# Optimization experiments

Measured on AMD Instinct MI355X. Metric: run time of the kernel, lower is better.

The kernel has to match this reference:

```python
import jax, jax.numpy as jnp
import numpy as np

B, T = 64, 2048
ENC_DIM, ATT_DIM, RNN_DIM, N_FILT, KSIZE, WIN = 512, 128, 1024, 32, 31, 32


def setup_inputs() -> dict:
    key = jax.random.key(0)
    ks = jax.random.split(key, 10)
    return {
        "attention_hidden_state": jax.random.normal(ks[0], (B, RNN_DIM), jnp.float32),
        "memory": jax.random.normal(ks[1], (B, T, ENC_DIM), jnp.float32),
        "processed_memory": jax.random.normal(ks[2], (B, T, ATT_DIM), jnp.float32),
        "attention_weights_cat": jax.random.uniform(ks[3], (B, 2, T), jnp.float32),
        "mask": jnp.zeros((B, T), jnp.bool_),
        "memory_lengths": jax.random.randint(ks[4], (B,), 0, T, jnp.int32),
        "current_pos": jax.random.uniform(ks[5], (B,), jnp.float32),
        "loc_conv_w": jax.random.normal(ks[6], (N_FILT, 2, KSIZE), jnp.float32) * 0.1,
        "loc_dense_w": jax.random.normal(ks[7], (ATT_DIM, N_FILT), jnp.float32) * 0.1,
        "query_w": jax.random.normal(ks[8], (ATT_DIM, RNN_DIM), jnp.float32) * 0.03,
        "v_w": jax.random.normal(ks[9], (1, ATT_DIM), jnp.float32) * 0.1,
        "pos_offset": jnp.zeros((1,), jnp.float32),
    }


def reference(attention_hidden_state, memory, processed_memory, attention_weights_cat,
              mask, memory_lengths, current_pos,
              loc_conv_w, loc_dense_w, query_w, v_w, pos_offset):
    Bn, Tn, _ = memory.shape
    pad = (KSIZE - 1) // 2
    # location conv: [B,2,T] -> [B,n_filters,T]
    conv = jax.lax.conv_general_dilated(
        attention_weights_cat, loc_conv_w, window_strides=(1,),
        padding=[(pad, pad)], dimension_numbers=("NCH", "OIH", "NCH"))
    # location dense + query projection + processed memory (fused add)
    processed = (jnp.einsum("bft,af->bta", conv, loc_dense_w)
                 + (attention_hidden_state @ query_w.T)[:, None, :]
                 + processed_memory)                      # [B,T,att_dim]
    alignment = jnp.tanh(processed) @ v_w[0]              # [B,T]
    # dynamic windowed mask around current_pos
    cp = current_pos + pos_offset[0]
    max_end = (memory_lengths - 1 - WIN).astype(cp.dtype)
    cp = jnp.minimum(jnp.maximum(cp, jnp.float32(WIN)), max_end)
    mask_start = jnp.round(jnp.maximum(cp - WIN, 0.0))
    mask_end = mask_start + 2 * WIN
    pos = jnp.arange(Tn, dtype=cp.dtype)
    pos_mask = (pos[None, :] >= mask_start[:, None]) & (pos[None, :] <= mask_end[:, None])
    full_mask = mask | ~pos_mask
    alignment = jnp.where(full_mask, jnp.float32(-1e9), alignment)
    attention_weights = jax.nn.softmax(alignment, axis=1)  # [B,T]
    attention_context = jnp.einsum("bt,btd->bd", attention_weights, memory)  # [B,enc_dim]
    new_pos = attention_weights @ jnp.arange(Tn, dtype=attention_weights.dtype)  # [B]
    return attention_context, attention_weights, new_pos
```

## Files before the change

### kernel.cpp

```cpp
#include <hip/hip_runtime.h>
#include <math.h>

#define Bn 64
#define Tn 2048
#define ENC 512
#define ATT 128
#define RNN 1024
#define NF 32
#define KS 31
#define WINR 32
#define WSZ 65
#define HALO 95

__global__ __launch_bounds__(256)
void attn_win_kernel(
    const float* __restrict__ hidden,
    const float* __restrict__ memory,
    const float* __restrict__ pmem,
    const float* __restrict__ cat,
    const unsigned char* __restrict__ mask,
    const int*  __restrict__ mlen,
    const float* __restrict__ cpos,
    const float* __restrict__ convw,
    const float* __restrict__ densew,
    const float* __restrict__ qw,
    const float* __restrict__ vw,
    const float* __restrict__ posoff,
    float* __restrict__ out)
{
    __shared__ float s_hidden[RNN];
    __shared__ float s_part[256];
    __shared__ float s_qproj[ATT];
    __shared__ float s_ldw[ATT * 33];
    __shared__ float s_cw[NF * 2 * KS];
    __shared__ float s_cat[2 * HALO];
    __shared__ float s_conv[WSZ * NF];
    __shared__ float s_align[WSZ];
    __shared__ float s_w[WSZ];

    const int b = blockIdx.x;
    const int tid = threadIdx.x;

    float cp = cpos[b] + posoff[0];
    float mend = (float)(mlen[b] - 1 - WINR);
    cp = fminf(fmaxf(cp, (float)WINR), mend);
    int s = (int)rintf(fmaxf(cp - (float)WINR, 0.0f));
    if (s < 0) s = 0;
    if (s > Tn - WSZ) s = Tn - WSZ;

    for (int i = tid; i < RNN; i += 256) s_hidden[i] = hidden[(size_t)b * RNN + i];
    for (int i = tid; i < ATT * NF; i += 256) {
        int a = i >> 5, f = i & 31;
        s_ldw[a * 33 + f] = densew[i];
    }
    for (int i = tid; i < NF * 2 * KS; i += 256) s_cw[i] = convw[i];
    for (int i = tid; i < 2 * HALO; i += 256) {
        int c = i / HALO, j = i - c * HALO;
        int t = s - (KS - 1) / 2 + j;
        float v = 0.0f;
        if (t >= 0 && t < Tn) v = cat[((size_t)b * 2 + c) * Tn + t];
        s_cat[c * HALO + j] = v;
    }
    __syncthreads();

    {
        int a = tid & 127, half = tid >> 7;
        const float4* q4 = (const float4*)(qw + (size_t)a * RNN + half * 512);
        const float4* h4 = (const float4*)(s_hidden + half * 512);
        float acc = 0.0f;
#pragma unroll 4
        for (int i = 0; i < 128; i++) {
            float4 q = q4[i], h = h4[i];
            acc += q.x * h.x + q.y * h.y + q.z * h.z + q.w * h.w;
        }
        s_part[tid] = acc;
    }
    __syncthreads();
    if (tid < ATT) s_qproj[tid] = s_part[tid] + s_part[tid + 128];

    for (int i = tid; i < WSZ * NF; i += 256) {
        int j = i >> 5, f = i & 31;
        const float* w0 = s_cw + f * 2 * KS;
        const float* c0 = s_cat + j;
        const float* c1 = s_cat + HALO + j;
        float acc = 0.0f;
#pragma unroll
        for (int k = 0; k < KS; k++) acc += c0[k] * w0[k] + c1[k] * w0[KS + k];
        s_conv[i] = acc;
    }
    __syncthreads();

    const int lane = tid & 63;
    const int wv = tid >> 6;
    const float va0 = vw[lane];
    const float va1 = vw[lane + 64];
    for (int j = wv; j < WSZ; j += 4) {
        int t = s + j;
        const float* pm = pmem + ((size_t)b * Tn + t) * ATT;
        const float* cv = s_conv + j * NF;
        const float* l0 = s_ldw + lane * 33;
        const float* l1 = s_ldw + (lane + 64) * 33;
        float x0 = s_qproj[lane] + pm[lane];
        float x1 = s_qproj[lane + 64] + pm[lane + 64];
#pragma unroll
        for (int f = 0; f < NF; f++) {
            float c = cv[f];
            x0 += c * l0[f];
            x1 += c * l1[f];
        }
        float val = tanhf(x0) * va0 + tanhf(x1) * va1;
        for (int off = 32; off > 0; off >>= 1) val += __shfl_down(val, off);
        if (lane == 0) {
            bool mk = mask[(size_t)b * Tn + t] != 0;
            s_align[j] = mk ? -1e9f : val;
        }
    }
    __syncthreads();

    if (tid < WSZ) {
        float m = -1e30f;
        for (int j = 0; j < WSZ; j++) m = fmaxf(m, s_align[j]);
        float sum = 0.0f;
        for (int j = 0; j < WSZ; j++) sum += expf(s_align[j] - m);
        s_w[tid] = expf(s_align[tid] - m) / sum;
    }
    __syncthreads();

    if (tid == 0) {
        float np = 0.0f;
        for (int j = 0; j < WSZ; j++) np += s_w[j] * (float)(s + j);
        out[(size_t)Bn * ENC + (size_t)Bn * Tn + b] = np;
    }

    {
        float4* wout = (float4*)(out + (size_t)Bn * ENC + (size_t)b * Tn);
        for (int i = tid; i < Tn / 4; i += 256) {
            float4 v;
            float* vv = (float*)&v;
#pragma unroll
            for (int q = 0; q < 4; q++) {
                int j = i * 4 + q - s;
                vv[q] = (j >= 0 && j < WSZ) ? s_w[j] : 0.0f;
            }
            wout[i] = v;
        }
    }

    {
        const float2* m2 = (const float2*)(memory + (size_t)b * Tn * ENC);
        float2 acc = make_float2(0.0f, 0.0f);
        for (int j = 0; j < WSZ; j++) {
            float wj = s_w[j];
            float2 mv = m2[(size_t)(s + j) * (ENC / 2) + tid];
            acc.x += wj * mv.x;
            acc.y += wj * mv.y;
        }
        ((float2*)out)[(size_t)b * (ENC / 2) + tid] = acc;
    }
}

extern "C" void kernel_launch(void* const* d_in, const int* in_sizes, int n_in,
                              void* d_out, int out_size, void* d_ws, size_t ws_size,
                              hipStream_t stream) {
    attn_win_kernel<<<Bn, 256, 0, stream>>>(
        (const float*)d_in[0],
        (const float*)d_in[1],
        (const float*)d_in[2],
        (const float*)d_in[3],
        (const unsigned char*)d_in[4],
        (const int*)d_in[5],
        (const float*)d_in[6],
        (const float*)d_in[7],
        (const float*)d_in[8],
        (const float*)d_in[9],
        (const float*)d_in[10],
        (const float*)d_in[11],
        (float*)d_out);
}
```

Baseline: 394.1 us.

## Split context gather into separate kernel and widen stage-one blocks

Splits the single per-batch kernel into two launches. The first computes alignment and softmax with 512 threads, prefetches the processed-memory window into shared memory with float4 loads, and writes the window weights and start index to workspace. The second computes the context over 256 blocks so that more CUs share the memory gather. This raises parallelism on a 64-block launch, at the cost of an extra kernel launch, a workspace round trip, and more shared memory in stage one.

```diff
diff --git a/kernel.cpp b/kernel.cpp
--- a/kernel.cpp
+++ b/kernel.cpp
@@ -11,11 +11,12 @@
 #define WINR 32
 #define WSZ 65
 #define HALO 95
-
-__global__ __launch_bounds__(256)
-void attn_win_kernel(
+#define WPAD 68
+
+
+__global__ __launch_bounds__(512)
+void attn_stage1(
     const float* __restrict__ hidden,
-    const float* __restrict__ memory,
     const float* __restrict__ pmem,
     const float* __restrict__ cat,
     const unsigned char* __restrict__ mask,
@@ -26,15 +27,18 @@
     const float* __restrict__ qw,
     const float* __restrict__ vw,
     const float* __restrict__ posoff,
-    float* __restrict__ out)
+    float* __restrict__ out,
+    float* __restrict__ ws_w,
+    int*   __restrict__ ws_s)
 {
     __shared__ float s_hidden[RNN];
-    __shared__ float s_part[256];
+    __shared__ float s_part[512];
     __shared__ float s_qproj[ATT];
     __shared__ float s_ldw[ATT * 33];
     __shared__ float s_cw[NF * 2 * KS];
     __shared__ float s_cat[2 * HALO];
     __shared__ float s_conv[WSZ * NF];
+    __shared__ float s_pm[WSZ * ATT];
     __shared__ float s_align[WSZ];
     __shared__ float s_w[WSZ];
 
@@ -48,13 +52,19 @@
     if (s < 0) s = 0;
     if (s > Tn - WSZ) s = Tn - WSZ;
 
-    for (int i = tid; i < RNN; i += 256) s_hidden[i] = hidden[(size_t)b * RNN + i];
-    for (int i = tid; i < ATT * NF; i += 256) {
+    for (int i = tid; i < RNN / 4; i += 512)
+        ((float4*)s_hidden)[i] = ((const float4*)(hidden + (size_t)b * RNN))[i];
+    {
+        const float4* pmw = (const float4*)(pmem + ((size_t)b * Tn + s) * ATT);
+        for (int i = tid; i < WSZ * ATT / 4; i += 512)
+            ((float4*)s_pm)[i] = pmw[i];
+    }
+    for (int i = tid; i < ATT * NF; i += 512) {
         int a = i >> 5, f = i & 31;
         s_ldw[a * 33 + f] = densew[i];
     }
-    for (int i = tid; i < NF * 2 * KS; i += 256) s_cw[i] = convw[i];
-    for (int i = tid; i < 2 * HALO; i += 256) {
+    for (int i = tid; i < NF * 2 * KS; i += 512) s_cw[i] = convw[i];
+    for (int i = tid; i < 2 * HALO; i += 512) {
         int c = i / HALO, j = i - c * HALO;
         int t = s - (KS - 1) / 2 + j;
         float v = 0.0f;
@@ -64,21 +74,22 @@
     __syncthreads();
 
     {
-        int a = tid & 127, half = tid >> 7;
-        const float4* q4 = (const float4*)(qw + (size_t)a * RNN + half * 512);
-        const float4* h4 = (const float4*)(s_hidden + half * 512);
+        int a = tid & 127, q = tid >> 7;
+        const float4* q4 = (const float4*)(qw + (size_t)a * RNN + q * 256);
+        const float4* h4 = (const float4*)(s_hidden + q * 256);
         float acc = 0.0f;
-#pragma unroll 4
-        for (int i = 0; i < 128; i++) {
-            float4 q = q4[i], h = h4[i];
-            acc += q.x * h.x + q.y * h.y + q.z * h.z + q.w * h.w;
+#pragma unroll 8
+        for (int i = 0; i < 64; i++) {
+            float4 x = q4[i], h = h4[i];
+            acc += x.x * h.x + x.y * h.y + x.z * h.z + x.w * h.w;
         }
         s_part[tid] = acc;
     }
     __syncthreads();
-    if (tid < ATT) s_qproj[tid] = s_part[tid] + s_part[tid + 128];
-
-    for (int i = tid; i < WSZ * NF; i += 256) {
+    if (tid < ATT)
+        s_qproj[tid] = s_part[tid] + s_part[tid + 128] + s_part[tid + 256] + s_part[tid + 384];
+
+    for (int i = tid; i < WSZ * NF; i += 512) {
         int j = i >> 5, f = i & 31;
         const float* w0 = s_cw + f * 2 * KS;
         const float* c0 = s_cat + j;
@@ -94,14 +105,13 @@
     const int wv = tid >> 6;
     const float va0 = vw[lane];
     const float va1 = vw[lane + 64];
-    for (int j = wv; j < WSZ; j += 4) {
-        int t = s + j;
-        const float* pm = pmem + ((size_t)b * Tn + t) * ATT;
+    for (int j = wv; j < WSZ; j += 8) {
+        const float* pmr = s_pm + j * ATT;
         const float* cv = s_conv + j * NF;
         const float* l0 = s_ldw + lane * 33;
         const float* l1 = s_ldw + (lane + 64) * 33;
-        float x0 = s_qproj[lane] + pm[lane];
-        float x1 = s_qproj[lane + 64] + pm[lane + 64];
+        float x0 = s_qproj[lane] + pmr[lane];
+        float x1 = s_qproj[lane + 64] + pmr[lane + 64];
 #pragma unroll
         for (int f = 0; f < NF; f++) {
             float c = cv[f];
@@ -111,7 +121,7 @@
         float val = tanhf(x0) * va0 + tanhf(x1) * va1;
         for (int off = 32; off > 0; off >>= 1) val += __shfl_down(val, off);
         if (lane == 0) {
-            bool mk = mask[(size_t)b * Tn + t] != 0;
+            bool mk = mask[(size_t)b * Tn + s + j] != 0;
             s_align[j] = mk ? -1e9f : val;
         }
     }
@@ -130,11 +140,13 @@
         float np = 0.0f;
         for (int j = 0; j < WSZ; j++) np += s_w[j] * (float)(s + j);
         out[(size_t)Bn * ENC + (size_t)Bn * Tn + b] = np;
-    }
+        ws_s[b] = s;
+    }
+    if (tid < WSZ) ws_w[b * WPAD + tid] = s_w[tid];
 
     {
         float4* wout = (float4*)(out + (size_t)Bn * ENC + (size_t)b * Tn);
-        for (int i = tid; i < Tn / 4; i += 256) {
+        for (int i = tid; i < Tn / 4; i += 512) {
             float4 v;
             float* vv = (float*)&v;
 #pragma unroll
@@ -145,26 +157,40 @@
             wout[i] = v;
         }
     }
-
-    {
-        const float2* m2 = (const float2*)(memory + (size_t)b * Tn * ENC);
-        float2 acc = make_float2(0.0f, 0.0f);
-        for (int j = 0; j < WSZ; j++) {
-            float wj = s_w[j];
-            float2 mv = m2[(size_t)(s + j) * (ENC / 2) + tid];
-            acc.x += wj * mv.x;
-            acc.y += wj * mv.y;
-        }
-        ((float2*)out)[(size_t)b * (ENC / 2) + tid] = acc;
-    }
+}
+
+__global__ __launch_bounds__(128)
+void attn_ctx(
+    const float* __restrict__ memory,
+    const float* __restrict__ ws_w,
+    const int*  __restrict__ ws_s,
+    float* __restrict__ out)
+{
+    __shared__ float s_w[WSZ];
+    __shared__ int s_sv;
+    const int b = blockIdx.x >> 2;
+    const int r = blockIdx.x & 3;
+    const int tid = threadIdx.x;
+    if (tid < WSZ) s_w[tid] = ws_w[b * WPAD + tid];
+    if (tid == 0) s_sv = ws_s[b];
+    __syncthreads();
+    const int s = s_sv;
+    const float* mb = memory + (size_t)b * Tn * ENC + r * 128 + tid;
+    float acc = 0.0f;
+#pragma unroll 5
+    for (int j = 0; j < WSZ; j++)
+        acc += s_w[j] * mb[(size_t)(s + j) * ENC];
+    out[(size_t)b * ENC + r * 128 + tid] = acc;
 }
 
 extern "C" void kernel_launch(void* const* d_in, const int* in_sizes, int n_in,
                               void* d_out, int out_size, void* d_ws, size_t ws_size,
                               hipStream_t stream) {
-    attn_win_kernel<<<Bn, 256, 0, stream>>>(
+    float* ws_w = (float*)d_ws;
+    int*   ws_s = (int*)((char*)d_ws + Bn * WPAD * 4);
+
+    attn_stage1<<<Bn, 512, 0, stream>>>(
         (const float*)d_in[0],
-        (const float*)d_in[1],
         (const float*)d_in[2],
         (const float*)d_in[3],
         (const unsigned char*)d_in[4],
@@ -175,5 +201,9 @@
         (const float*)d_in[9],
         (const float*)d_in[10],
         (const float*)d_in[11],
-        (float*)d_out);
+        (float*)d_out, ws_w, ws_s);
+
+    attn_ctx<<<Bn * 4, 128, 0, stream>>>(
+        (const float*)d_in[1],
+        ws_w, ws_s, (float*)d_out);
 }
```

New measurement: 381.2 us. 1.03x faster.
